# Kernel optimization log

Hardware: AMD Instinct MI355X
Metric: run time of the kernel (lower is better)

The kernel has to match this reference:

```python
import jax, jax.numpy as jnp
import numpy as np

B, T, HIDDEN, QLR = 1, 2560, 7168, 1536
N_HEADS, HEAD_DIM, ROPE_DIM, TOPK = 64, 128, 64, 2048
LN_EPS = 1e-6


def _rope(x, cos, sin):
    # non-interleaved (half-split) rotary: pairs are (x[i], x[i+d/2])
    d = x.shape[-1] // 2
    x1, x2 = x[..., :d], x[..., d:]
    return jnp.concatenate([x1 * cos - x2 * sin, x1 * sin + x2 * cos], axis=-1)


def setup_inputs() -> dict:
    key = jax.random.key(0)
    ks = jax.random.split(key, 6)
    x = jax.random.normal(ks[0], (B, T, HIDDEN), dtype=jnp.float32)
    qr = jax.random.normal(ks[1], (B, T, QLR), dtype=jnp.float32)
    # rope tables (theta = 10000)
    inv_freq = 1.0 / (10000.0 ** (jnp.arange(0, ROPE_DIM, 2, dtype=jnp.float32) / ROPE_DIM))
    angles = jnp.arange(T, dtype=jnp.float32)[:, None] * inv_freq[None, :]  # [T, 32]
    freqs_cos = jnp.cos(angles)
    freqs_sin = jnp.sin(angles)
    # causal additive mask
    i = jnp.arange(T)
    mask = jnp.where(i[None, :, None] >= i[None, None, :], 0.0, -1e9).astype(jnp.float32)  # [1,T,T]
    # params (torch Linear stored transposed so y = x @ W)
    s = 0.02
    wq_b = jax.random.normal(ks[2], (QLR, N_HEADS * HEAD_DIM), dtype=jnp.float32) * s
    wk_w = jax.random.normal(ks[3], (HIDDEN, HEAD_DIM), dtype=jnp.float32) * s
    k_gamma = jnp.ones((HEAD_DIM,), dtype=jnp.float32)
    k_beta = jnp.zeros((HEAD_DIM,), dtype=jnp.float32)
    wproj = jax.random.normal(ks[4], (HIDDEN, N_HEADS), dtype=jnp.float32) * s
    return {"x": x, "qr": qr, "freqs_cos": freqs_cos, "freqs_sin": freqs_sin,
            "mask": mask, "wq_b": wq_b, "wk_w": wk_w, "k_gamma": k_gamma,
            "k_beta": k_beta, "wproj": wproj}


def reference(x, qr, freqs_cos, freqs_sin, mask, wq_b, wk_w, k_gamma, k_beta, wproj):
    bsz, seqlen, _ = x.shape
    # queries
    q = (qr @ wq_b).reshape(bsz, seqlen, N_HEADS, HEAD_DIM)
    q_pe, q_nope = q[..., :ROPE_DIM], q[..., ROPE_DIM:]
    q_pe = _rope(q_pe, freqs_cos[None, :, None, :], freqs_sin[None, :, None, :])
    q = jnp.concatenate([q_pe, q_nope], axis=-1)  # [B,T,H,D]
    # keys: layernorm(wk(x))
    k = x @ wk_w  # [B,T,D]
    mu = jnp.mean(k, axis=-1, keepdims=True)
    var = jnp.mean(jnp.square(k - mu), axis=-1, keepdims=True)
    k = (k - mu) / jnp.sqrt(var + LN_EPS) * k_gamma + k_beta
    k_pe, k_nope = k[..., :ROPE_DIM], k[..., ROPE_DIM:]
    k_pe = _rope(k_pe, freqs_cos[None, :, :], freqs_sin[None, :, :])
    k = jnp.concatenate([k_pe, k_nope], axis=-1)  # [B,S,D]
    # per-head weights
    weights = (x @ wproj) * (N_HEADS ** -0.5) * (HEAD_DIM ** -0.5)  # [B,T,H]
    # relu score + weighted head reduce
    logits = jax.nn.relu(jnp.einsum('bthd,bsd->btsh', q, k))  # [B,T,S,H]
    index_score = jnp.einsum('btsh,bth->bts', logits, weights) + mask
    # top-k + scatter mask
    kk = min(TOPK, seqlen)
    _, topk_idx = jax.lax.top_k(index_score, kk)  # [B,T,K]
    index_mask = jnp.full((bsz, seqlen, seqlen), -1e9, dtype=jnp.float32)
    bi = jnp.arange(bsz)[:, None, None]
    ti = jnp.arange(seqlen)[None, :, None]
    index_mask = index_mask.at[bi, ti, topk_idx].set(0.0)
    return index_mask
```

## Files before the change

kernel.cpp:

```cpp
#include <hip/hip_runtime.h>
#include <cstdint>

#define T_SEQ   2560
#define HID     7168
#define QLRD    1536
#define NHEAD   64
#define HDIM    128
#define TOPK    2048
#define T0SEL   2048
#define NSEL    512

#define QHOFF 0
#define QLOFF 2097152
#define KOFF  4194304
#define WOFF  4521984
#define KHOFF 4554752
#define KLOFF 4718592
#define SOFF  5242880

typedef _Float16 half8 __attribute__((ext_vector_type(8)));
typedef _Float16 half4v __attribute__((ext_vector_type(4)));
typedef float    floatx16 __attribute__((ext_vector_type(16)));

__global__ __launch_bounds__(384) void kw_kernel(
        const float* __restrict__ x, const float* __restrict__ wk,
        const float* __restrict__ wp, float* __restrict__ Pk,
        float* __restrict__ Pw, long pkstride, long pwstride, int klen) {
    const int t0 = blockIdx.x * 64;
    const int chunk = blockIdx.y;
    const int k0 = chunk * klen;
    const int kl = min(klen, HID - k0);
    const int steps = kl >> 5;
    float* pk = Pk + (size_t)chunk * pkstride;
    float* pw = Pw + (size_t)chunk * pwstride;

    const int tid = threadIdx.x;
    const int lane = tid & 63;
    const int wv = tid >> 6;
    const int wt = wv / 3;
    const int wn2 = wv % 3;
    const int l31 = lane & 31;
    const int kb = (lane >> 5) * 8;

    __shared__ __align__(16) _Float16 Ah[64 * 40];
    __shared__ __align__(16) _Float16 Al[64 * 40];
    __shared__ __align__(16) _Float16 Bh[192 * 40];
    __shared__ __align__(16) _Float16 Bl[192 * 40];

    const int am = tid >> 2;
    const int ak = (tid & 3) * 8;
    const int bkr = (tid / 48) * 4;
    const int bnr = (tid % 48) * 4;

    const float* aptr = x + (size_t)(t0 + am) * HID + k0 + ak;
    const float* bsrc; int bld, bcol;
    if (bnr < 128) { bsrc = wk; bld = 128; bcol = bnr; }
    else           { bsrc = wp; bld = 64;  bcol = bnr - 128; }
    const float* bptr = bsrc + (size_t)(k0 + bkr) * bld + bcol;

    float4 pa0, pa1;
    if (tid < 256) { pa0 = *(const float4*)(aptr + 0); pa1 = *(const float4*)(aptr + 4); }
    float4 pb0 = *(const float4*)(bptr + 0 * (size_t)bld);
    float4 pb1 = *(const float4*)(bptr + 1 * (size_t)bld);
    float4 pb2 = *(const float4*)(bptr + 2 * (size_t)bld);
    float4 pb3 = *(const float4*)(bptr + 3 * (size_t)bld);

    floatx16 Z = {0.f,0.f,0.f,0.f,0.f,0.f,0.f,0.f,0.f,0.f,0.f,0.f,0.f,0.f,0.f,0.f};
    floatx16 Chh0 = Z, Chl0 = Z, Clh0 = Z;
    floatx16 Chh1 = Z, Chl1 = Z, Clh1 = Z;

    for (int ks = 0; ks < steps; ++ks) {
        __syncthreads();
        if (tid < 256) {
            float av[8];
            *(float4*)&av[0] = pa0; *(float4*)&av[4] = pa1;
            half8 ha, la;
#pragma unroll
            for (int i = 0; i < 8; ++i) {
                float v = av[i];
                _Float16 hi = (_Float16)v;
                ha[i] = hi;
                la[i] = (_Float16)(v - (float)hi);
            }
            *(half8*)&Ah[am * 40 + ak] = ha;
            *(half8*)&Al[am * 40 + ak] = la;
        }
        {
            float bv[4][4];
            *(float4*)&bv[0][0] = pb0; *(float4*)&bv[1][0] = pb1;
            *(float4*)&bv[2][0] = pb2; *(float4*)&bv[3][0] = pb3;
#pragma unroll
            for (int j = 0; j < 4; ++j) {
                half4v hb, lb;
#pragma unroll
                for (int i = 0; i < 4; ++i) {
                    float v = bv[i][j] * 64.0f;
                    _Float16 hi = (_Float16)v;
                    hb[i] = hi;
                    lb[i] = (_Float16)(v - (float)hi);
                }
                *(half4v*)&Bh[(bnr + j) * 40 + bkr] = hb;
                *(half4v*)&Bl[(bnr + j) * 40 + bkr] = lb;
            }
        }
        __syncthreads();
        if (ks + 1 < steps) {
            aptr += 32; bptr += (size_t)32 * bld;
            if (tid < 256) { pa0 = *(const float4*)(aptr + 0); pa1 = *(const float4*)(aptr + 4); }
            pb0 = *(const float4*)(bptr + 0 * (size_t)bld);
            pb1 = *(const float4*)(bptr + 1 * (size_t)bld);
            pb2 = *(const float4*)(bptr + 2 * (size_t)bld);
            pb3 = *(const float4*)(bptr + 3 * (size_t)bld);
        }
#pragma unroll
        for (int c = 0; c < 2; ++c) {
            const int ka = c * 16 + kb;
            half8 ah  = *(const half8*)&Ah[(wt * 32 + l31) * 40 + ka];
            half8 al  = *(const half8*)&Al[(wt * 32 + l31) * 40 + ka];
            half8 bh0 = *(const half8*)&Bh[(wn2 * 64 + l31) * 40 + ka];
            half8 bl0 = *(const half8*)&Bl[(wn2 * 64 + l31) * 40 + ka];
            half8 bh1 = *(const half8*)&Bh[(wn2 * 64 + 32 + l31) * 40 + ka];
            half8 bl1 = *(const half8*)&Bl[(wn2 * 64 + 32 + l31) * 40 + ka];
            Chh0 = __builtin_amdgcn_mfma_f32_32x32x16_f16(ah, bh0, Chh0, 0, 0, 0);
            Chl0 = __builtin_amdgcn_mfma_f32_32x32x16_f16(ah, bl0, Chl0, 0, 0, 0);
            Clh0 = __builtin_amdgcn_mfma_f32_32x32x16_f16(al, bh0, Clh0, 0, 0, 0);
            Chh1 = __builtin_amdgcn_mfma_f32_32x32x16_f16(ah, bh1, Chh1, 0, 0, 0);
            Chl1 = __builtin_amdgcn_mfma_f32_32x32x16_f16(ah, bl1, Chl1, 0, 0, 0);
            Clh1 = __builtin_amdgcn_mfma_f32_32x32x16_f16(al, bh1, Clh1, 0, 0, 0);
        }
    }

    const int rbase = wt * 32 + 4 * (lane >> 5);
#pragma unroll
    for (int r = 0; r < 16; ++r) {
        int trow = t0 + rbase + (r & 3) + 8 * (r >> 2);
        float v0 = ((Chh0[r] + Chl0[r]) + Clh0[r]) * 0.015625f;
        float v1 = ((Chh1[r] + Chl1[r]) + Clh1[r]) * 0.015625f;
        int c0 = wn2 * 64 + l31;
        if (wn2 < 2) {
            pk[(size_t)trow * 128 + c0] = v0;
            pk[(size_t)trow * 128 + c0 + 32] = v1;
        } else if (trow >= T0SEL) {
            pw[(size_t)(trow - T0SEL) * 64 + c0 - 128] = v0;
            pw[(size_t)(trow - T0SEL) * 64 + c0 - 96] = v1;
        }
    }
}

__global__ void reduce2_kernel(float* __restrict__ dk, const float* __restrict__ sk,
                               long kstr, float* __restrict__ dw,
                               const float* __restrict__ sw, long wstr, int nchunk) {
    int i = blockIdx.x * 256 + threadIdx.x;
    if (i < 327680) {
        float s = sk[i];
        for (int c = 1; c < nchunk; ++c) s += sk[(size_t)c * kstr + i];
        dk[i] = s;
    } else {
        int j = i - 327680;
        float s = sw[j];
        for (int c = 1; c < nchunk; ++c) s += sw[(size_t)c * wstr + j];
        dw[j] = s;
    }
}

__global__ void lnrope_kernel(const float* __restrict__ fcos, const float* __restrict__ fsin,
                              const float* __restrict__ gamma, const float* __restrict__ beta,
                              const float* __restrict__ Kbuf, float* __restrict__ Wbuf,
                              _Float16* __restrict__ KhG, _Float16* __restrict__ KlG) {
#pragma clang fp contract(off)
    const int s = blockIdx.x;
    const int d = threadIdx.x;
    __shared__ float red[128];
    __shared__ float kn[128];
    float kv = Kbuf[(size_t)s * 128 + d];
    red[d] = kv;
    __syncthreads();
    for (int off = 64; off > 0; off >>= 1) {
        if (d < off) red[d] += red[d + off];
        __syncthreads();
    }
    float mu = red[0] / 128.0f;
    __syncthreads();
    float dv = kv - mu;
    red[d] = dv * dv;
    __syncthreads();
    for (int off = 64; off > 0; off >>= 1) {
        if (d < off) red[d] += red[d + off];
        __syncthreads();
    }
    float var = red[0] / 128.0f;
    float nrm = dv / sqrtf(var + 1e-6f);
    nrm = nrm * gamma[d] + beta[d];
    kn[d] = nrm;
    __syncthreads();
    float o;
    if (d < 64) {
        int p = d & 31;
        float c = fcos[s * 32 + p], sn = fsin[s * 32 + p];
        if (d < 32) o = kn[d] * c - kn[d + 32] * sn;
        else        o = kn[d - 32] * sn + kn[d] * c;
    } else {
        o = kn[d];
    }
    _Float16 hi = (_Float16)o;
    _Float16 lo = (_Float16)(o - (float)hi);
    KhG[(size_t)s * 128 + d] = hi;
    KlG[(size_t)s * 128 + d] = lo;
    if (s >= T0SEL && d < 64) {
        Wbuf[(size_t)(s - T0SEL) * 64 + d] *= (0.125f * 0.08838834764831845f);
    }
}

__global__ __launch_bounds__(256, 3) void q_kernel(
        const float* __restrict__ qr, const float* __restrict__ wqb,
        const float* __restrict__ fcos, const float* __restrict__ fsin,
        _Float16* __restrict__ QhG, _Float16* __restrict__ QlG) {
    const int bx = blockIdx.x;
    const int head = blockIdx.y;
    const int tid = threadIdx.x;
    const int lane = tid & 63;
    const int wv = tid >> 6;
    const int wt = wv >> 1, wn = wv & 1;
    const int l31 = lane & 31;
    const int kb = (lane >> 5) * 8;

    __shared__ __align__(16) _Float16 Ah[64 * 40];
    __shared__ __align__(16) _Float16 Al[64 * 40];
    __shared__ __align__(16) _Float16 Bh[128 * 40];
    __shared__ __align__(16) _Float16 Bl[128 * 40];

    const int am = tid >> 2;
    const int ak = (tid & 3) * 8;
    const int bn = (tid & 31) * 4;
    const int bk = (tid >> 5) * 4;

    const float* aptr = qr + (size_t)(T0SEL + bx * 64 + am) * QLRD + ak;
    const float* bptr = wqb + (size_t)bk * 8192 + head * 128 + bn;

    float4 pa0 = *(const float4*)(aptr + 0);
    float4 pa1 = *(const float4*)(aptr + 4);
    float4 pb0 = *(const float4*)(bptr + 0 * 8192);
    float4 pb1 = *(const float4*)(bptr + 1 * 8192);
    float4 pb2 = *(const float4*)(bptr + 2 * 8192);
    float4 pb3 = *(const float4*)(bptr + 3 * 8192);

    floatx16 Z = {0.f,0.f,0.f,0.f,0.f,0.f,0.f,0.f,0.f,0.f,0.f,0.f,0.f,0.f,0.f,0.f};
    floatx16 Chh0 = Z, Chl0 = Z, Clh0 = Z;
    floatx16 Chh1 = Z, Chl1 = Z, Clh1 = Z;

    for (int ks = 0; ks < QLRD / 32; ++ks) {
        __syncthreads();
        {
            float av[8];
            *(float4*)&av[0] = pa0; *(float4*)&av[4] = pa1;
            half8 ha, la;
#pragma unroll
            for (int i = 0; i < 8; ++i) {
                float v = av[i];
                _Float16 hi = (_Float16)v;
                ha[i] = hi;
                la[i] = (_Float16)(v - (float)hi);
            }
            *(half8*)&Ah[am * 40 + ak] = ha;
            *(half8*)&Al[am * 40 + ak] = la;
        }
        {
            float bv[4][4];
            *(float4*)&bv[0][0] = pb0; *(float4*)&bv[1][0] = pb1;
            *(float4*)&bv[2][0] = pb2; *(float4*)&bv[3][0] = pb3;
#pragma unroll
            for (int j = 0; j < 4; ++j) {
                half4v hb, lb;
#pragma unroll
                for (int i = 0; i < 4; ++i) {
                    float v = bv[i][j] * 64.0f;
                    _Float16 hi = (_Float16)v;
                    hb[i] = hi;
                    lb[i] = (_Float16)(v - (float)hi);
                }
                *(half4v*)&Bh[(bn + j) * 40 + bk] = hb;
                *(half4v*)&Bl[(bn + j) * 40 + bk] = lb;
            }
        }
        __syncthreads();
        if (ks + 1 < QLRD / 32) {
            aptr += 32; bptr += (size_t)32 * 8192;
            pa0 = *(const float4*)(aptr + 0);
            pa1 = *(const float4*)(aptr + 4);
            pb0 = *(const float4*)(bptr + 0 * 8192);
            pb1 = *(const float4*)(bptr + 1 * 8192);
            pb2 = *(const float4*)(bptr + 2 * 8192);
            pb3 = *(const float4*)(bptr + 3 * 8192);
        }
#pragma unroll
        for (int c = 0; c < 2; ++c) {
            const int ka = c * 16 + kb;
            half8 ah = *(const half8*)&Ah[(wt * 32 + l31) * 40 + ka];
            half8 al = *(const half8*)&Al[(wt * 32 + l31) * 40 + ka];
            half8 bh0 = *(const half8*)&Bh[(wn * 64 + l31) * 40 + ka];
            half8 bl0 = *(const half8*)&Bl[(wn * 64 + l31) * 40 + ka];
            half8 bh1 = *(const half8*)&Bh[(wn * 64 + 32 + l31) * 40 + ka];
            half8 bl1 = *(const half8*)&Bl[(wn * 64 + 32 + l31) * 40 + ka];
            Chh0 = __builtin_amdgcn_mfma_f32_32x32x16_f16(ah, bh0, Chh0, 0, 0, 0);
            Chl0 = __builtin_amdgcn_mfma_f32_32x32x16_f16(ah, bl0, Chl0, 0, 0, 0);
            Clh0 = __builtin_amdgcn_mfma_f32_32x32x16_f16(al, bh0, Clh0, 0, 0, 0);
            Chh1 = __builtin_amdgcn_mfma_f32_32x32x16_f16(ah, bh1, Chh1, 0, 0, 0);
            Chl1 = __builtin_amdgcn_mfma_f32_32x32x16_f16(ah, bl1, Chl1, 0, 0, 0);
            Clh1 = __builtin_amdgcn_mfma_f32_32x32x16_f16(al, bh1, Clh1, 0, 0, 0);
        }
    }

    {
#pragma clang fp contract(off)
        const int tbase = bx * 64 + wt * 32 + 4 * (lane >> 5);
#pragma unroll
        for (int r = 0; r < 16; ++r) {
            int tl = tbase + (r & 3) + 8 * (r >> 2);
            float v0 = ((Chh0[r] + Chl0[r]) + Clh0[r]) * 0.015625f;
            float v1 = ((Chh1[r] + Chl1[r]) + Clh1[r]) * 0.015625f;
            float o0, o1;
            if (wn == 0) {
                int tg = T0SEL + tl;
                float c = fcos[tg * 32 + l31];
                float s = fsin[tg * 32 + l31];
                o0 = v0 * c - v1 * s;
                o1 = v0 * s + v1 * c;
            } else {
                o0 = v0; o1 = v1;
            }
            int d0 = wn * 64 + l31;
            size_t off = (size_t)head * 65536 + (size_t)tl * 128;
            _Float16 h0 = (_Float16)o0;
            _Float16 h1 = (_Float16)o1;
            QhG[off + d0] = h0;
            QlG[off + d0] = (_Float16)(o0 - (float)h0);
            QhG[off + d0 + 32] = h1;
            QlG[off + d0 + 32] = (_Float16)(o1 - (float)h1);
        }
    }
}

__global__ __launch_bounds__(256) void score_kernel(
        const _Float16* __restrict__ Qh, const _Float16* __restrict__ Ql,
        const _Float16* __restrict__ Kh, const _Float16* __restrict__ Kl,
        const float* __restrict__ Wbuf, float* __restrict__ S0,
        float* __restrict__ S1, int hcnt) {
    const int bid = blockIdx.x;
    const int tt0 = (bid & 15) * 32;
    const int s0  = (bid >> 4) * 128;
    const int hb  = blockIdx.y * hcnt;
    float* __restrict__ dst = blockIdx.y ? S1 : S0;
    const int tid = threadIdx.x;
    const int wv  = tid >> 6;
    const int lane = tid & 63;
    const int l31 = lane & 31;
    const int kb  = (lane >> 5) * 8;

    __shared__ __align__(16) _Float16 AhA[32 * 136];
    __shared__ __align__(16) _Float16 AlA[32 * 136];
    __shared__ __align__(16) _Float16 AhB[32 * 136];
    __shared__ __align__(16) _Float16 AlB[32 * 136];
    __shared__ float WsT[64 * 36];

    half8 Bh[8], Bl[8];
    {
        const int srow = s0 + wv * 32 + l31;
        const _Float16* kh = Kh + (size_t)srow * 128 + kb;
        const _Float16* kl = Kl + (size_t)srow * 128 + kb;
#pragma unroll
        for (int c = 0; c < 8; ++c) {
            Bh[c] = *(const half8*)(kh + c * 16);
            Bl[c] = *(const half8*)(kl + c * 16);
        }
    }
#pragma unroll
    for (int r = 0; r < 8; ++r) {
        int idx = tid + 256 * r;
        int row = idx >> 6, h = idx & 63;
        WsT[h * 36 + row] = Wbuf[(size_t)(tt0 + row) * 64 + h];
    }

    const int srow0 = tid >> 4;
    const int scc0  = (tid & 15) * 8;
    const int srow1 = srow0 + 16;
    const int scc1  = scc0;

    const _Float16* qhp = Qh + (size_t)hb * 65536 + (size_t)tt0 * 128;
    const _Float16* qlp = Ql + (size_t)hb * 65536 + (size_t)tt0 * 128;

    half8 sh0 = *(const half8*)&qhp[srow0 * 128 + scc0];
    half8 sh1 = *(const half8*)&qhp[srow1 * 128 + scc1];
    half8 sl0 = *(const half8*)&qlp[srow0 * 128 + scc0];
    half8 sl1 = *(const half8*)&qlp[srow1 * 128 + scc1];
    *(half8*)&AhA[srow0 * 136 + scc0] = sh0;
    *(half8*)&AhA[srow1 * 136 + scc1] = sh1;
    *(half8*)&AlA[srow0 * 136 + scc0] = sl0;
    *(half8*)&AlA[srow1 * 136 + scc1] = sl1;
    qhp += 65536; qlp += 65536;
    sh0 = *(const half8*)&qhp[srow0 * 128 + scc0];
    sh1 = *(const half8*)&qhp[srow1 * 128 + scc1];
    sl0 = *(const half8*)&qlp[srow0 * 128 + scc0];
    sl1 = *(const half8*)&qlp[srow1 * 128 + scc1];
    __builtin_amdgcn_sched_barrier(0);
    __syncthreads();

    float S[16];
#pragma unroll
    for (int r = 0; r < 16; ++r) S[r] = 0.0f;

#define SCORE_COMPUTE(AH, AL, HIDX)                                            \
    {                                                                          \
        floatx16 C0 = {0.f,0.f,0.f,0.f,0.f,0.f,0.f,0.f,                        \
                       0.f,0.f,0.f,0.f,0.f,0.f,0.f,0.f};                       \
        floatx16 C2 = C0, C3 = C0;                                             \
        __builtin_amdgcn_s_setprio(1);                                         \
        _Pragma("unroll")                                                      \
        for (int c = 0; c < 8; ++c) {                                          \
            half8 a_h = *(const half8*)&AH[l31 * 136 + c * 16 + kb];           \
            half8 a_l = *(const half8*)&AL[l31 * 136 + c * 16 + kb];           \
            C0 = __builtin_amdgcn_mfma_f32_32x32x16_f16(a_h, Bh[c], C0, 0, 0, 0); \
            C2 = __builtin_amdgcn_mfma_f32_32x32x16_f16(a_h, Bl[c], C2, 0, 0, 0); \
            C3 = __builtin_amdgcn_mfma_f32_32x32x16_f16(a_l, Bh[c], C3, 0, 0, 0); \
        }                                                                      \
        __builtin_amdgcn_s_setprio(0);                                         \
        const float* wb = &WsT[(HIDX) * 36 + 4 * (lane >> 5)];                 \
        float4 w0 = *(const float4*)(wb + 0);                                  \
        float4 w1 = *(const float4*)(wb + 8);                                  \
        float4 w2 = *(const float4*)(wb + 16);                                 \
        float4 w3 = *(const float4*)(wb + 24);                                 \
        float w[16] = {w0.x, w0.y, w0.z, w0.w, w1.x, w1.y, w1.z, w1.w,         \
                       w2.x, w2.y, w2.z, w2.w, w3.x, w3.y, w3.z, w3.w};        \
        _Pragma("unroll")                                                      \
        for (int r = 0; r < 16; ++r) {                                         \
            float L = (C0[r] + C2[r]) + C3[r];                                 \
            S[r] += w[r] * fmaxf(L, 0.0f);                                     \
        }                                                                      \
    }

    for (int h = 0; h < hcnt; h += 2) {
        SCORE_COMPUTE(AhA, AlA, hb + h)
        *(half8*)&AhB[srow0 * 136 + scc0] = sh0;
        *(half8*)&AhB[srow1 * 136 + scc1] = sh1;
        *(half8*)&AlB[srow0 * 136 + scc0] = sl0;
        *(half8*)&AlB[srow1 * 136 + scc1] = sl1;
        qhp += 65536; qlp += 65536;
        sh0 = *(const half8*)&qhp[srow0 * 128 + scc0];
        sh1 = *(const half8*)&qhp[srow1 * 128 + scc1];
        sl0 = *(const half8*)&qlp[srow0 * 128 + scc0];
        sl1 = *(const half8*)&qlp[srow1 * 128 + scc1];
        __builtin_amdgcn_sched_barrier(0);
        __syncthreads();

        SCORE_COMPUTE(AhB, AlB, hb + h + 1)
        *(half8*)&AhA[srow0 * 136 + scc0] = sh0;
        *(half8*)&AhA[srow1 * 136 + scc1] = sh1;
        *(half8*)&AlA[srow0 * 136 + scc0] = sl0;
        *(half8*)&AlA[srow1 * 136 + scc1] = sl1;
        qhp += 65536; qlp += 65536;
        sh0 = *(const half8*)&qhp[srow0 * 128 + scc0];
        sh1 = *(const half8*)&qhp[srow1 * 128 + scc1];
        sl0 = *(const half8*)&qlp[srow0 * 128 + scc0];
        sl1 = *(const half8*)&qlp[srow1 * 128 + scc1];
        __builtin_amdgcn_sched_barrier(0);
        __syncthreads();
    }
#undef SCORE_COMPUTE

    const int scol = s0 + wv * 32 + l31;
#pragma unroll
    for (int r = 0; r < 16; ++r) {
        int trow = tt0 + (r & 3) + 8 * (r >> 2) + 4 * (lane >> 5);
        dst[(size_t)trow * 2560 + scol] = S[r] + 0.0f;
    }
}

__global__ void finalize_kernel(float* __restrict__ out, const float* __restrict__ S1) {
    const int row_id = blockIdx.x;
    const int tid = threadIdx.x;

    if (row_id < T0SEL) {
        const float4 zero4 = make_float4(0.0f, 0.0f, 0.0f, 0.0f);
        const float4 neg4 = make_float4(-1000000000.0f, -1000000000.0f,
                                        -1000000000.0f, -1000000000.0f);
        for (int i = tid; i < T_SEQ / 4; i += 256) {
            *(float4*)&out[(size_t)row_id * T_SEQ + i * 4] = (i * 4 < TOPK) ? zero4 : neg4;
        }
        return;
    }

    const int t = row_id;
    const int n = t + 1;
    float* row = out + (size_t)t * T_SEQ;
    const float* s1p = S1 ? (S1 + (size_t)(t - T0SEL) * T_SEQ) : nullptr;

    __shared__ unsigned U[T_SEQ];
    __shared__ int hist[256];
    __shared__ int aux[256];
    __shared__ unsigned sh_prefix;
    __shared__ int sh_kneed;

    for (int i = tid; i < T_SEQ; i += 256) {
        unsigned u = 0u;
        if (i < n) {
            float sc = row[i];
            if (s1p) sc += s1p[i];
            int b = __float_as_int(sc);
            u = (b < 0) ? ~((unsigned)b) : (((unsigned)b) | 0x80000000u);
        }
        U[i] = u;
    }
    if (tid == 0) { sh_prefix = 0u; sh_kneed = TOPK; }
    __syncthreads();

    for (int pass = 0; pass < 4; ++pass) {
        const int shift = 24 - 8 * pass;
        const unsigned himask = (pass == 0) ? 0u : (0xFFFFFFFFu << (shift + 8));
        hist[tid] = 0;
        __syncthreads();
        const unsigned pre = sh_prefix;
        const int kneed = sh_kneed;
        for (int i = tid; i < T_SEQ; i += 256) {
            unsigned u = U[i];
            if ((u & himask) == pre) atomicAdd(&hist[(u >> shift) & 255], 1);
        }
        __syncthreads();
        aux[tid] = hist[tid];
        __syncthreads();
        for (int off = 1; off < 256; off <<= 1) {
            int a = (tid + off < 256) ? aux[tid + off] : 0;
            __syncthreads();
            aux[tid] += a;
            __syncthreads();
        }
        int above = (tid < 255) ? aux[tid + 1] : 0;
        if (above < kneed && kneed <= aux[tid]) {
            sh_prefix = pre | (((unsigned)tid) << shift);
            sh_kneed = kneed - above;
        }
        __syncthreads();
    }
    const unsigned theta = sh_prefix;
    const int r = sh_kneed;

    const int s_lo = tid * 10, s_hi = s_lo + 10;
    int c = 0;
    for (int s = s_lo; s < s_hi; ++s) c += (U[s] == theta);
    aux[tid] = c;
    __syncthreads();
    for (int off = 1; off < 256; off <<= 1) {
        int a = (tid >= off) ? aux[tid - off] : 0;
        __syncthreads();
        aux[tid] += a;
        __syncthreads();
    }
    int rank = aux[tid] - c;
    for (int s = s_lo; s < s_hi; ++s) {
        unsigned u = U[s];
        bool sel = (u > theta) || (u == theta && rank < r);
        if (u == theta) ++rank;
        row[s] = sel ? 0.0f : -1000000000.0f;
    }
}

extern "C" void kernel_launch(void* const* d_in, const int* in_sizes, int n_in,
                              void* d_out, int out_size, void* d_ws, size_t ws_size,
                              hipStream_t stream) {
    (void)in_sizes; (void)n_in; (void)out_size;
    const float* x     = (const float*)d_in[0];
    const float* qr    = (const float*)d_in[1];
    const float* fcos  = (const float*)d_in[2];
    const float* fsin  = (const float*)d_in[3];
    const float* wqb   = (const float*)d_in[5];
    const float* wk    = (const float*)d_in[6];
    const float* gamma = (const float*)d_in[7];
    const float* beta  = (const float*)d_in[8];
    const float* wp    = (const float*)d_in[9];

    float* out  = (float*)d_out;
    float* Kbuf = out + KOFF;
    float* Wbuf = out + WOFF;
    float* Sbuf = out + SOFF;
    _Float16* QhG = (_Float16*)(out + QHOFF);
    _Float16* QlG = (_Float16*)(out + QLOFF);
    _Float16* KhG = (_Float16*)(out + KHOFF);
    _Float16* KlG = (_Float16*)(out + KLOFF);

    const size_t need = (size_t)(6 * 327680 + 6 * 32768) * 4;
    int nchunk; int klen; float *Pk, *Pw; long pkstride, pwstride;
    if (ws_size >= need) {
        nchunk = 6; klen = 1216;
        Pk = (float*)d_ws;            pkstride = 327680;
        Pw = (float*)d_ws + 1966080;  pwstride = 32768;
    } else {
        nchunk = 2; klen = 3584;
        Pk = out + KOFF;  pkstride = 360448;
        Pw = out + WOFF;  pwstride = 360448;
    }

    const size_t s1_need = (size_t)NSEL * T_SEQ * sizeof(float);
    float* S1 = (ws_size >= s1_need) ? (float*)d_ws : nullptr;

    kw_kernel<<<dim3(40, nchunk), 384, 0, stream>>>(x, wk, wp, Pk, Pw, pkstride, pwstride, klen);
    reduce2_kernel<<<1408, 256, 0, stream>>>(Kbuf, Pk, pkstride, Wbuf, Pw, pwstride, nchunk);
    lnrope_kernel<<<T_SEQ, 128, 0, stream>>>(fcos, fsin, gamma, beta, Kbuf, Wbuf, KhG, KlG);
    q_kernel<<<dim3(8, 64), 256, 0, stream>>>(qr, wqb, fcos, fsin, QhG, QlG);
    if (S1) {
        score_kernel<<<dim3(320, 2), 256, 0, stream>>>(QhG, QlG, KhG, KlG, Wbuf, Sbuf, S1, 32);
    } else {
        score_kernel<<<dim3(320, 1), 256, 0, stream>>>(QhG, QlG, KhG, KlG, Wbuf, Sbuf, nullptr, 64);
    }
    finalize_kernel<<<T_SEQ, 256, 0, stream>>>(out, S1);
}
```

Measured before the change: 408.8 us.

## Double-buffer q_kernel global prefetch and use lighter LDS-only barriers

Replaces __syncthreads with a barrier that waits only on LDS counters, so outstanding global prefetches are not drained at each sync in kw, q and score kernels. q_kernel now keeps two register sets of prefetched tiles, giving two steps of global-load lookahead. It also raises MFMA priority with s_setprio and swaps grid axes so consecutive blocks share the same qr rows. Launch bounds drop to 2 waves-per-EU minimum to make room for the extra registers, at the cost of possible occupancy loss.

Result: faster. 393.5 us (-3.7%).

```diff
diff --git a/kernel.cpp b/kernel.cpp
--- a/kernel.cpp
+++ b/kernel.cpp
@@ -21,6 +21,11 @@
 typedef _Float16 half8 __attribute__((ext_vector_type(8)));
 typedef _Float16 half4v __attribute__((ext_vector_type(4)));
 typedef float    floatx16 __attribute__((ext_vector_type(16)));
+
+__device__ __forceinline__ void lds_barrier() {
+    asm volatile("s_waitcnt lgkmcnt(0)" ::: "memory");
+    __builtin_amdgcn_s_barrier();
+}
 
 __global__ __launch_bounds__(384) void kw_kernel(
         const float* __restrict__ x, const float* __restrict__ wk,
@@ -70,7 +75,7 @@
     floatx16 Chh1 = Z, Chl1 = Z, Clh1 = Z;
 
     for (int ks = 0; ks < steps; ++ks) {
-        __syncthreads();
+        lds_barrier();
         if (tid < 256) {
             float av[8];
             *(float4*)&av[0] = pa0; *(float4*)&av[4] = pa1;
@@ -103,7 +108,7 @@
                 *(half4v*)&Bl[(bnr + j) * 40 + bkr] = lb;
             }
         }
-        __syncthreads();
+        lds_barrier();
         if (ks + 1 < steps) {
             aptr += 32; bptr += (size_t)32 * bld;
             if (tid < 256) { pa0 = *(const float4*)(aptr + 0); pa1 = *(const float4*)(aptr + 4); }
@@ -112,6 +117,7 @@
             pb2 = *(const float4*)(bptr + 2 * (size_t)bld);
             pb3 = *(const float4*)(bptr + 3 * (size_t)bld);
         }
+        __builtin_amdgcn_sched_barrier(0);
 #pragma unroll
         for (int c = 0; c < 2; ++c) {
             const int ka = c * 16 + kb;
@@ -211,12 +217,12 @@
     }
 }
 
-__global__ __launch_bounds__(256, 3) void q_kernel(
+__global__ __launch_bounds__(256, 2) void q_kernel(
         const float* __restrict__ qr, const float* __restrict__ wqb,
         const float* __restrict__ fcos, const float* __restrict__ fsin,
         _Float16* __restrict__ QhG, _Float16* __restrict__ QlG) {
-    const int bx = blockIdx.x;
-    const int head = blockIdx.y;
+    const int head = blockIdx.x;
+    const int bx = blockIdx.y;
     const int tid = threadIdx.x;
     const int lane = tid & 63;
     const int wv = tid >> 6;
@@ -234,81 +240,101 @@
     const int bn = (tid & 31) * 4;
     const int bk = (tid >> 5) * 4;
 
-    const float* aptr = qr + (size_t)(T0SEL + bx * 64 + am) * QLRD + ak;
-    const float* bptr = wqb + (size_t)bk * 8192 + head * 128 + bn;
-
-    float4 pa0 = *(const float4*)(aptr + 0);
-    float4 pa1 = *(const float4*)(aptr + 4);
-    float4 pb0 = *(const float4*)(bptr + 0 * 8192);
-    float4 pb1 = *(const float4*)(bptr + 1 * 8192);
-    float4 pb2 = *(const float4*)(bptr + 2 * 8192);
-    float4 pb3 = *(const float4*)(bptr + 3 * 8192);
+    const float* aB = qr + (size_t)(T0SEL + bx * 64 + am) * QLRD + ak;
+    const float* bB = wqb + (size_t)bk * 8192 + head * 128 + bn;
+
+    float4 paA0, paA1, pbA0, pbA1, pbA2, pbA3;
+    float4 paB0, paB1, pbB0, pbB1, pbB2, pbB3;
+
+#define QLOADSET(PA0,PA1,PB0,PB1,PB2,PB3,KK) do {                              \
+    const float* ap_ = aB + (size_t)(KK) * 32;                                 \
+    const float* bp_ = bB + (size_t)(KK) * 32 * 8192;                          \
+    PA0 = *(const float4*)(ap_ + 0);                                           \
+    PA1 = *(const float4*)(ap_ + 4);                                           \
+    PB0 = *(const float4*)(bp_ + 0 * 8192);                                    \
+    PB1 = *(const float4*)(bp_ + 1 * 8192);                                    \
+    PB2 = *(const float4*)(bp_ + 2 * 8192);                                    \
+    PB3 = *(const float4*)(bp_ + 3 * 8192);                                    \
+} while (0)
+
+#define QCONVERT(PA0,PA1,PB0,PB1,PB2,PB3) do {                                 \
+    float av[8];                                                               \
+    *(float4*)&av[0] = PA0; *(float4*)&av[4] = PA1;                            \
+    half8 ha, la;                                                              \
+    _Pragma("unroll")                                                          \
+    for (int i = 0; i < 8; ++i) {                                              \
+        float v = av[i];                                                       \
+        _Float16 hi = (_Float16)v;                                             \
+        ha[i] = hi;                                                            \
+        la[i] = (_Float16)(v - (float)hi);                                     \
+    }                                                                          \
+    *(half8*)&Ah[am * 40 + ak] = ha;                                           \
+    *(half8*)&Al[am * 40 + ak] = la;                                           \
+    float bv[4][4];                                                            \
+    *(float4*)&bv[0][0] = PB0; *(float4*)&bv[1][0] = PB1;                      \
+    *(float4*)&bv[2][0] = PB2; *(float4*)&bv[3][0] = PB3;                      \
+    _Pragma("unroll")                                                          \
+    for (int j = 0; j < 4; ++j) {                                              \
+        half4v hb, lb;                                                         \
+        _Pragma("unroll")                                                      \
+        for (int i = 0; i < 4; ++i) {                                          \
+            float v = bv[i][j] * 64.0f;                                        \
+            _Float16 hi = (_Float16)v;                                         \
+            hb[i] = hi;                                                        \
+            lb[i] = (_Float16)(v - (float)hi);                                 \
+        }                                                                      \
+        *(half4v*)&Bh[(bn + j) * 40 + bk] = hb;                                \
+        *(half4v*)&Bl[(bn + j) * 40 + bk] = lb;                                \
+    }                                                                          \
+} while (0)
+
+#define QMFMA() do {                                                           \
+    __builtin_amdgcn_s_setprio(1);                                             \
+    _Pragma("unroll")                                                          \
+    for (int c = 0; c < 2; ++c) {                                              \
+        const int ka = c * 16 + kb;                                            \
+        half8 ah = *(const half8*)&Ah[(wt * 32 + l31) * 40 + ka];              \
+        half8 al = *(const half8*)&Al[(wt * 32 + l31) * 40 + ka];              \
+        half8 bh0 = *(const half8*)&Bh[(wn * 64 + l31) * 40 + ka];             \
+        half8 bl0 = *(const half8*)&Bl[(wn * 64 + l31) * 40 + ka];             \
+        half8 bh1 = *(const half8*)&Bh[(wn * 64 + 32 + l31) * 40 + ka];        \
+        half8 bl1 = *(const half8*)&Bl[(wn * 64 + 32 + l31) * 40 + ka];        \
+        Chh0 = __builtin_amdgcn_mfma_f32_32x32x16_f16(ah, bh0, Chh0, 0, 0, 0); \
+        Chl0 = __builtin_amdgcn_mfma_f32_32x32x16_f16(ah, bl0, Chl0, 0, 0, 0); \
+        Clh0 = __builtin_amdgcn_mfma_f32_32x32x16_f16(al, bh0, Clh0, 0, 0, 0); \
+        Chh1 = __builtin_amdgcn_mfma_f32_32x32x16_f16(ah, bh1, Chh1, 0, 0, 0); \
+        Chl1 = __builtin_amdgcn_mfma_f32_32x32x16_f16(ah, bl1, Chl1, 0, 0, 0); \
+        Clh1 = __builtin_amdgcn_mfma_f32_32x32x16_f16(al, bh1, Clh1, 0, 0, 0); \
+    }                                                                          \
+    __builtin_amdgcn_s_setprio(0);                                             \
+} while (0)
 
     floatx16 Z = {0.f,0.f,0.f,0.f,0.f,0.f,0.f,0.f,0.f,0.f,0.f,0.f,0.f,0.f,0.f,0.f};
     floatx16 Chh0 = Z, Chl0 = Z, Clh0 = Z;
     floatx16 Chh1 = Z, Chl1 = Z, Clh1 = Z;
 
-    for (int ks = 0; ks < QLRD / 32; ++ks) {
-        __syncthreads();
-        {
-            float av[8];
-            *(float4*)&av[0] = pa0; *(float4*)&av[4] = pa1;
-            half8 ha, la;
-#pragma unroll
-            for (int i = 0; i < 8; ++i) {
-                float v = av[i];
-                _Float16 hi = (_Float16)v;
-                ha[i] = hi;
-                la[i] = (_Float16)(v - (float)hi);
-            }
-            *(half8*)&Ah[am * 40 + ak] = ha;
-            *(half8*)&Al[am * 40 + ak] = la;
-        }
-        {
-            float bv[4][4];
-            *(float4*)&bv[0][0] = pb0; *(float4*)&bv[1][0] = pb1;
-            *(float4*)&bv[2][0] = pb2; *(float4*)&bv[3][0] = pb3;
-#pragma unroll
-            for (int j = 0; j < 4; ++j) {
-                half4v hb, lb;
-#pragma unroll
-                for (int i = 0; i < 4; ++i) {
-                    float v = bv[i][j] * 64.0f;
-                    _Float16 hi = (_Float16)v;
-                    hb[i] = hi;
-                    lb[i] = (_Float16)(v - (float)hi);
-                }
-                *(half4v*)&Bh[(bn + j) * 40 + bk] = hb;
-                *(half4v*)&Bl[(bn + j) * 40 + bk] = lb;
-            }
-        }
-        __syncthreads();
-        if (ks + 1 < QLRD / 32) {
-            aptr += 32; bptr += (size_t)32 * 8192;
-            pa0 = *(const float4*)(aptr + 0);
-            pa1 = *(const float4*)(aptr + 4);
-            pb0 = *(const float4*)(bptr + 0 * 8192);
-            pb1 = *(const float4*)(bptr + 1 * 8192);
-            pb2 = *(const float4*)(bptr + 2 * 8192);
-            pb3 = *(const float4*)(bptr + 3 * 8192);
-        }
-#pragma unroll
-        for (int c = 0; c < 2; ++c) {
-            const int ka = c * 16 + kb;
-            half8 ah = *(const half8*)&Ah[(wt * 32 + l31) * 40 + ka];
-            half8 al = *(const half8*)&Al[(wt * 32 + l31) * 40 + ka];
-            half8 bh0 = *(const half8*)&Bh[(wn * 64 + l31) * 40 + ka];
-            half8 bl0 = *(const half8*)&Bl[(wn * 64 + l31) * 40 + ka];
-            half8 bh1 = *(const half8*)&Bh[(wn * 64 + 32 + l31) * 40 + ka];
-            half8 bl1 = *(const half8*)&Bl[(wn * 64 + 32 + l31) * 40 + ka];
-            Chh0 = __builtin_amdgcn_mfma_f32_32x32x16_f16(ah, bh0, Chh0, 0, 0, 0);
-            Chl0 = __builtin_amdgcn_mfma_f32_32x32x16_f16(ah, bl0, Chl0, 0, 0, 0);
-            Clh0 = __builtin_amdgcn_mfma_f32_32x32x16_f16(al, bh0, Clh0, 0, 0, 0);
-            Chh1 = __builtin_amdgcn_mfma_f32_32x32x16_f16(ah, bh1, Chh1, 0, 0, 0);
-            Chl1 = __builtin_amdgcn_mfma_f32_32x32x16_f16(ah, bl1, Chl1, 0, 0, 0);
-            Clh1 = __builtin_amdgcn_mfma_f32_32x32x16_f16(al, bh1, Clh1, 0, 0, 0);
-        }
-    }
+    const int steps = QLRD / 32;
+    QLOADSET(paA0, paA1, pbA0, pbA1, pbA2, pbA3, 0);
+    QLOADSET(paB0, paB1, pbB0, pbB1, pbB2, pbB3, 1);
+
+    for (int ks = 0; ks < steps; ks += 2) {
+        lds_barrier();
+        QCONVERT(paA0, paA1, pbA0, pbA1, pbA2, pbA3);
+        lds_barrier();
+        QLOADSET(paA0, paA1, pbA0, pbA1, pbA2, pbA3, min(ks + 2, steps - 1));
+        __builtin_amdgcn_sched_barrier(0);
+        QMFMA();
+
+        lds_barrier();
+        QCONVERT(paB0, paB1, pbB0, pbB1, pbB2, pbB3);
+        lds_barrier();
+        QLOADSET(paB0, paB1, pbB0, pbB1, pbB2, pbB3, min(ks + 3, steps - 1));
+        __builtin_amdgcn_sched_barrier(0);
+        QMFMA();
+    }
+#undef QLOADSET
+#undef QCONVERT
+#undef QMFMA
 
     {
 #pragma clang fp contract(off)
@@ -402,7 +428,7 @@
     sl0 = *(const half8*)&qlp[srow0 * 128 + scc0];
     sl1 = *(const half8*)&qlp[srow1 * 128 + scc1];
     __builtin_amdgcn_sched_barrier(0);
-    __syncthreads();
+    lds_barrier();
 
     float S[16];
 #pragma unroll
@@ -449,7 +475,7 @@
         sl0 = *(const half8*)&qlp[srow0 * 128 + scc0];
         sl1 = *(const half8*)&qlp[srow1 * 128 + scc1];
         __builtin_amdgcn_sched_barrier(0);
-        __syncthreads();
+        lds_barrier();
 
         SCORE_COMPUTE(AhB, AlB, hb + h + 1)
         *(half8*)&AhA[srow0 * 136 + scc0] = sh0;
@@ -462,7 +488,7 @@
         sl0 = *(const half8*)&qlp[srow0 * 128 + scc0];
         sl1 = *(const half8*)&qlp[srow1 * 128 + scc1];
         __builtin_amdgcn_sched_barrier(0);
-        __syncthreads();
+        lds_barrier();
     }
 #undef SCORE_COMPUTE
 
@@ -603,7 +629,7 @@
     kw_kernel<<<dim3(40, nchunk), 384, 0, stream>>>(x, wk, wp, Pk, Pw, pkstride, pwstride, klen);
     reduce2_kernel<<<1408, 256, 0, stream>>>(Kbuf, Pk, pkstride, Wbuf, Pw, pwstride, nchunk);
     lnrope_kernel<<<T_SEQ, 128, 0, stream>>>(fcos, fsin, gamma, beta, Kbuf, Wbuf, KhG, KlG);
-    q_kernel<<<dim3(8, 64), 256, 0, stream>>>(qr, wqb, fcos, fsin, QhG, QlG);
+    q_kernel<<<dim3(64, 8), 256, 0, stream>>>(qr, wqb, fcos, fsin, QhG, QlG);
     if (S1) {
         score_kernel<<<dim3(320, 2), 256, 0, stream>>>(QhG, QlG, KhG, KlG, Wbuf, Sbuf, S1, 32);
     } else {
```
